# Kernel tuning notes

Measured on AMD Instinct MI355X. Metric: run time of the kernel, lower is better.

## Reference

```python
import jax, jax.numpy as jnp
import numpy as np

N_HEADS = 16
HEAD_SIZE = 64
N_EMB = 1024
BLOCK = 2048
B, T = 2, 2048

def setup_inputs() -> dict:
    key = jax.random.key(0)
    ks = jax.random.split(key, 6)
    s = 0.02
    x = jax.random.normal(ks[0], (B, T, N_EMB), dtype=jnp.float32)
    # per-head projection weights, stacked: [H, C, hs] (no bias, per module)
    Wq = jax.random.normal(ks[1], (N_HEADS, N_EMB, HEAD_SIZE), dtype=jnp.float32) * s
    Wk = jax.random.normal(ks[2], (N_HEADS, N_EMB, HEAD_SIZE), dtype=jnp.float32) * s
    Wv = jax.random.normal(ks[3], (N_HEADS, N_EMB, HEAD_SIZE), dtype=jnp.float32) * s
    # output projection: Linear(n_heads*head_size -> n_embedding), with bias
    Wo = jax.random.normal(ks[4], (N_HEADS * HEAD_SIZE, N_EMB), dtype=jnp.float32) * s
    bo = jax.random.normal(ks[5], (N_EMB,), dtype=jnp.float32) * s
    return {"x": x, "Wq": Wq, "Wk": Wk, "Wv": Wv, "Wo": Wo, "bo": bo}

def reference(x, Wq, Wk, Wv, Wo, bo):
    # x: [B,T,C]; projections per head -> [B,H,T,hs]
    q = jnp.einsum('btc,hcd->bhtd', x, Wq)
    k = jnp.einsum('btc,hcd->bhtd', x, Wk)
    v = jnp.einsum('btc,hcd->bhtd', x, Wv)
    scale = 1.0 / jnp.sqrt(jnp.asarray(HEAD_SIZE, dtype=x.dtype))
    scores = jnp.einsum('bhtd,bhsd->bhts', q, k) * scale  # [B,H,T,T]
    Tq = x.shape[1]
    causal = jnp.tril(jnp.ones((Tq, Tq), dtype=bool))
    scores = jnp.where(causal, scores, jnp.asarray(-jnp.inf, dtype=scores.dtype))
    attn = jax.nn.softmax(scores, axis=-1)  # dropout in eval mode (identity)
    out = jnp.einsum('bhts,bhsd->bhtd', attn, v)  # [B,H,T,hs]
    # concat heads along last dim (matches torch.cat order over head list)
    out = out.transpose(0, 2, 1, 3).reshape(x.shape[0], Tq, N_HEADS * HEAD_SIZE)
    return out @ Wo + bo
```

## Files before the change

kernel.cpp:

```cpp
#include <hip/hip_runtime.h>


typedef short v8s __attribute__((ext_vector_type(8)));
typedef float v4f __attribute__((ext_vector_type(4)));

#define DEVI __device__ __forceinline__

#define B_SZ 2
#define T_SEQ 2048
#define NH 16
#define HS 64
#define CEMB 1024
#define MROWS (B_SZ * T_SEQ)
#define KSZ 1024
#define SCALE_Q 0.18033688011112042f

DEVI unsigned short f2bf(float f) {
  union { float f; unsigned u; } c; c.f = f;
  unsigned u = c.u;
  unsigned r = (u + 0x7FFFu + ((u >> 16) & 1u)) >> 16;
  return (unsigned short)r;
}

DEVI float exp2_fast(float x) {
  float r;
  asm("v_exp_f32 %0, %1" : "=v"(r) : "v"(x));
  return r;
}

DEVI unsigned cvt_pk_bf16(float lo, float hi) {
  unsigned r;
  asm("v_cvt_pk_bf16_f32 %0, %1, %2" : "=v"(r) : "v"(lo), "v"(hi));
  return r;
}

DEVI void gload_lds16(const void* g, void* l) {
  __builtin_amdgcn_global_load_lds(
      (const __attribute__((address_space(1))) void*)g,
      (__attribute__((address_space(3))) void*)l, 16, 0, 0);
}

DEVI int xcd_swz(int bid, int nwg) {
  int q = nwg >> 3;
  return (bid & 7) * q + (bid >> 3);
}

__global__ __launch_bounds__(256, 4) void prep_kernel(
    const float* __restrict__ x, const float* __restrict__ Wq,
    const float* __restrict__ Wk, const float* __restrict__ Wv,
    const float* __restrict__ Wo, unsigned short* __restrict__ xb,
    unsigned short* __restrict__ Wt, unsigned short* __restrict__ Wot) {
  int bid = blockIdx.x;
  if (bid < 2048) {
    int i = bid * 2048 + threadIdx.x * 8;
    float4 a = *(const float4*)(x + i);
    float4 b = *(const float4*)(x + i + 4);
    ushort4 o0, o1;
    o0.x = f2bf(a.x); o0.y = f2bf(a.y); o0.z = f2bf(a.z); o0.w = f2bf(a.w);
    o1.x = f2bf(b.x); o1.y = f2bf(b.y); o1.z = f2bf(b.z); o1.w = f2bf(b.w);
    *(ushort4*)(xb + i) = o0;
    *(ushort4*)(xb + i + 4) = o1;
    return;
  }
  __shared__ float tile[32][33];
  const float* in; unsigned short* out;
  int C, bx, by;
  if (bid < 5120) {
    int b2 = bid - 2048;
    int widx = b2 >> 10, rem = b2 & 1023;
    in = (widx == 0 ? Wq : (widx == 1 ? Wk : Wv));
    int z = rem >> 6;
    bx = rem & 1; by = (rem >> 1) & 31;
    C = 64;
    in += (size_t)z * 1024 * 64;
    out = Wt + ((size_t)widx << 20) + (size_t)z * 1024 * 64;
  } else {
    int rem = bid - 5120;
    C = 1024;
    bx = rem & 31; by = rem >> 5;
    in = Wo; out = Wot;
  }
  int c0 = bx * 32, r0 = by * 32;
  int tx = threadIdx.x & 31, ty = threadIdx.x >> 5;
#pragma unroll
  for (int j = 0; j < 4; ++j)
    tile[ty + j * 8][tx] = in[(size_t)(r0 + ty + j * 8) * C + c0 + tx];
  __syncthreads();
#pragma unroll
  for (int j = 0; j < 4; ++j)
    out[(size_t)(c0 + ty + j * 8) * 1024 + r0 + tx] = f2bf(tile[tx][ty + j * 8]);
}

template <int MODE>
__global__ __launch_bounds__(256, 3) void gemm_bt(
    const unsigned short* __restrict__ A, const unsigned short* __restrict__ Bt,
    void* __restrict__ Cout, const float* __restrict__ bias, int nbx) {
  __shared__ __align__(16) unsigned short As[3][128 * 32];
  __shared__ __align__(16) unsigned short Bs[3][128 * 32];

  const int tid = threadIdx.x;
  const int lane = tid & 63, w = tid >> 6;
  const int wm = w >> 1, wn = w & 1;
  const int lr = lane & 15, lg = lane >> 4;

  const int wg = xcd_swz(blockIdx.x, gridDim.x);
  const int mb = (wg / nbx) * 128, nb = (wg % nbx) * 128;

  v4f acc[4][4];
  v4f zero = {0.f, 0.f, 0.f, 0.f};
#pragma unroll
  for (int i = 0; i < 4; ++i)
#pragma unroll
    for (int j = 0; j < 4; ++j) acc[i][j] = zero;

  const int srow = lane >> 2;
  const int sgcol = ((lane & 3) ^ (srow & 3)) * 8;
  const unsigned short* gA = A + (size_t)(mb + w * 32 + srow) * KSZ + sgcol;
  const unsigned short* gB = Bt + (size_t)(nb + w * 32 + srow) * KSZ + sgcol;
  unsigned short* lA = &As[0][0] + w * 1024;
  unsigned short* lB = &Bs[0][0] + w * 1024;

#define STAGE_G(buf, kb)                                        \
  do {                                                          \
    gload_lds16(gA + (kb), lA + (buf) * 4096);                  \
    gload_lds16(gA + (kb) + 16 * KSZ, lA + (buf) * 4096 + 512); \
    gload_lds16(gB + (kb), lB + (buf) * 4096);                  \
    gload_lds16(gB + (kb) + 16 * KSZ, lB + (buf) * 4096 + 512); \
  } while (0)

  STAGE_G(0, 0);
  STAGE_G(1, 32);
  STAGE_G(2, 64);

  const int NT = KSZ / 32;
  for (int t = 0; t < NT; ++t) {
    asm volatile("s_waitcnt vmcnt(8)" ::: "memory");
    __builtin_amdgcn_s_barrier();

    const int buf = t % 3;
    v8s af[4], bfr[4];
#pragma unroll
    for (int i = 0; i < 4; ++i) {
      int ra = wm * 64 + i * 16 + lr, rb = wn * 64 + i * 16 + lr;
      af[i]  = *(const v8s*)&As[buf][ra * 32 + ((lg ^ (lr & 3)) << 3)];
      bfr[i] = *(const v8s*)&Bs[buf][rb * 32 + ((lg ^ (lr & 3)) << 3)];
    }
#pragma unroll
    for (int i = 0; i < 4; ++i)
#pragma unroll
      for (int j = 0; j < 4; ++j)
        acc[i][j] = __builtin_amdgcn_mfma_f32_16x16x32_bf16(af[i], bfr[j], acc[i][j], 0, 0, 0);

    asm volatile("s_waitcnt lgkmcnt(0)" ::: "memory");
    __builtin_amdgcn_s_barrier();
    if (t + 3 < NT) STAGE_G(buf, (t + 3) * 32);
  }
#undef STAGE_G

#pragma unroll
  for (int i = 0; i < 4; ++i) {
    int mrow0 = mb + wm * 64 + i * 16 + lg * 4;
#pragma unroll
    for (int j = 0; j < 4; ++j) {
      int ncol = nb + wn * 64 + j * 16 + lr;
      if (MODE == 0) {
        int p = ncol >> 10, rem = ncol & 1023, h = rem >> 6, d = rem & 63;
        float sc = (p == 0) ? SCALE_Q : 1.0f;
        unsigned short* out = (unsigned short*)Cout;
#pragma unroll
        for (int r = 0; r < 4; ++r) {
          int mrow = mrow0 + r;
          int b = mrow >> 11, t = mrow & 2047;
          size_t off;
          if (p < 2)
            off = ((size_t)((p * B_SZ + b) * NH + h) * T_SEQ + t) * HS + d;
          else
            off = (size_t)(2 * B_SZ * NH) * T_SEQ * HS +
                  ((size_t)(b * NH + h) * HS + d) * T_SEQ + t;
          out[off] = f2bf(acc[i][j][r] * sc);
        }
      } else {
        float* out = (float*)Cout;
        float bv = bias[ncol];
#pragma unroll
        for (int r = 0; r < 4; ++r)
          out[(size_t)(mrow0 + r) * CEMB + ncol] = acc[i][j][r] + bv;
      }
    }
  }
}

__global__ __launch_bounds__(512, 4) void attn_kernel(
    const unsigned short* __restrict__ Qg, const unsigned short* __restrict__ Kg,
    const unsigned short* __restrict__ Vtg, unsigned short* __restrict__ Yg) {
  __shared__ __align__(16) unsigned char lds[32 * 1024];
  unsigned char* KsB = lds;
  unsigned char* VtB = lds + 16384;

  const int tid = threadIdx.x;
  const int lane = tid & 63, w = tid >> 6;
  const int lr = lane & 15, lg = lane >> 4;
  const int qc = 15 - (blockIdx.x >> 5);
  const int bh = blockIdx.x & 31;

  const unsigned short* Qbase = Qg + (size_t)bh * T_SEQ * HS;
  const unsigned short* Kbase = Kg + (size_t)bh * T_SEQ * HS;
  const unsigned short* Vtbase = Vtg + (size_t)bh * T_SEQ * HS;

  const int ks_row = tid >> 3, ks_cb = tid & 7;
  const int kLds0 = ks_row * 128 + ((ks_cb ^ (ks_row & 7)) << 4);
  const unsigned short* Kg0 = Kbase + ks_row * HS + ks_cb * 8;
  const int vs_d = tid >> 4, vs_m = tid & 15;
  const int vLds0 = vs_d * 256 + ((vs_m ^ (vs_d & 15)) << 4);
  const int vbt = ((vs_m >> 2) << 4) + ((vs_m & 3) << 2);
  const unsigned short* Vg0 = Vtbase + (size_t)vs_d * T_SEQ + vbt;

  v8s qA[2];
  {
    const unsigned short* qrow = Qbase + (size_t)(qc * 128 + w * 16 + lr) * HS;
    qA[0] = *(const v8s*)(qrow + lg * 8);
    qA[1] = *(const v8s*)(qrow + 32 + lg * 8);
  }

  v4f O[4];
  v4f zero = {0.f, 0.f, 0.f, 0.f};
#pragma unroll
  for (int d = 0; d < 4; ++d) O[d] = zero;
  float mrun = -1e30f, lrun = 0.f;

  int4 gK0 = *(const int4*)(Kg0);
  int4 gK1 = *(const int4*)(Kg0 + 4096);
  int2 vlo0 = *(const int2*)(Vg0);
  int2 vhi0 = *(const int2*)(Vg0 + 64);
  int2 vlo1 = *(const int2*)(Vg0 + 32 * T_SEQ);
  int2 vhi1 = *(const int2*)(Vg0 + 32 * T_SEQ + 64);

  for (int t = 0; t <= qc; ++t) {
    __syncthreads();
    *(int4*)(KsB + kLds0) = gK0;
    *(int4*)(KsB + kLds0 + 8192) = gK1;
    {
      int4 v0; v0.x = vlo0.x; v0.y = vlo0.y; v0.z = vhi0.x; v0.w = vhi0.y;
      int4 v1; v1.x = vlo1.x; v1.y = vlo1.y; v1.z = vhi1.x; v1.w = vhi1.y;
      *(int4*)(VtB + vLds0) = v0;
      *(int4*)(VtB + vLds0 + 8192) = v1;
    }
    __syncthreads();
    if (t < qc) {
      const unsigned short* kp = Kg0 + (t + 1) * (128 * HS);
      gK0 = *(const int4*)kp;
      gK1 = *(const int4*)(kp + 4096);
      const unsigned short* vp = Vg0 + (t + 1) * 128;
      vlo0 = *(const int2*)(vp);
      vhi0 = *(const int2*)(vp + 64);
      vlo1 = *(const int2*)(vp + 32 * T_SEQ);
      vhi1 = *(const int2*)(vp + 32 * T_SEQ + 64);
    }

    const int cflim = (t == qc) ? w : 7;

    v4f S[8];
    __builtin_amdgcn_s_setprio(1);
#pragma unroll
    for (int cf = 0; cf < 8; ++cf) {
      if (cf <= cflim) {
        S[cf] = zero;
#pragma unroll
        for (int ks = 0; ks < 2; ++ks) {
          int srow = cf * 16 + lr;
          v8s kb = *(const v8s*)(KsB + srow * 128 +
                                 ((((ks << 2) + lg) ^ (lr & 7)) << 4));
          S[cf] = __builtin_amdgcn_mfma_f32_16x16x32_bf16(kb, qA[ks], S[cf], 0, 0, 0);
        }
      } else {
        S[cf] = (v4f){-1e30f, -1e30f, -1e30f, -1e30f};
      }
    }
    __builtin_amdgcn_s_setprio(0);

    if (t == qc) {
#pragma unroll
      for (int cf = 0; cf < 8; ++cf)
        if (cf == w) {
#pragma unroll
          for (int r = 0; r < 4; ++r)
            if (lg * 4 + r > lr) S[cf][r] = -1e30f;
        }
    }

    float mx = -1e30f;
#pragma unroll
    for (int cf = 0; cf < 8; ++cf)
#pragma unroll
      for (int r = 0; r < 4; ++r) mx = fmaxf(mx, S[cf][r]);
    mx = fmaxf(mx, __shfl_xor(mx, 16));
    mx = fmaxf(mx, __shfl_xor(mx, 32));

    if (!__all(mx - mrun <= 8.0f)) {
      float mn = fmaxf(mrun, mx);
      float alpha = exp2_fast(mrun - mn);
      mrun = mn;
      lrun *= alpha;
#pragma unroll
      for (int df = 0; df < 4; ++df)
#pragma unroll
        for (int r = 0; r < 4; ++r) O[df][r] *= alpha;
    }

    float sum = 0.f;
#pragma unroll
    for (int cf = 0; cf < 8; ++cf)
#pragma unroll
      for (int r = 0; r < 4; ++r) {
        float p = exp2_fast(S[cf][r] - mrun);
        S[cf][r] = p;
        sum += p;
      }
    sum += __shfl_xor(sum, 16);
    sum += __shfl_xor(sum, 32);
    lrun += sum;

    unsigned pk0[8], pk1[8];
#pragma unroll
    for (int cf = 0; cf < 8; ++cf) {
      pk0[cf] = cvt_pk_bf16(S[cf][0], S[cf][1]);
      pk1[cf] = cvt_pk_bf16(S[cf][2], S[cf][3]);
    }

    __builtin_amdgcn_s_setprio(1);
#pragma unroll
    for (int c = 0; c < 4; ++c) {
      if (t != qc || c <= w) {
        union { unsigned u[4]; v8s s; } pu;
        pu.u[0] = pk0[c]; pu.u[1] = pk1[c];
        pu.u[2] = pk0[c + 4]; pu.u[3] = pk1[c + 4];
        v8s pa = pu.s;
#pragma unroll
        for (int df = 0; df < 4; ++df) {
          int d = df * 16 + lr;
          v8s va = *(const v8s*)(VtB + d * 256 +
                                 ((((c << 2) + lg) ^ lr) << 4));
          O[df] = __builtin_amdgcn_mfma_f32_16x16x32_bf16(va, pa, O[df], 0, 0, 0);
        }
      }
    }
    __builtin_amdgcn_s_setprio(0);
  }

  float invl = 1.0f / lrun;
  int tq = qc * 128 + w * 16 + lr;
  int b = bh >> 4, h = bh & 15;
  size_t ybase = ((size_t)b * T_SEQ + tq) * (NH * HS) + h * 64;
#pragma unroll
  for (int df = 0; df < 4; ++df) {
    ushort4 o4;
    o4.x = f2bf(O[df][0] * invl);
    o4.y = f2bf(O[df][1] * invl);
    o4.z = f2bf(O[df][2] * invl);
    o4.w = f2bf(O[df][3] * invl);
    *(ushort4*)(Yg + ybase + df * 16 + lg * 4) = o4;
  }
}

extern "C" void kernel_launch(void* const* d_in, const int* in_sizes, int n_in,
                              void* d_out, int out_size, void* d_ws, size_t ws_size,
                              hipStream_t stream) {
  (void)in_sizes; (void)n_in; (void)out_size; (void)ws_size;
  const float* x  = (const float*)d_in[0];
  const float* Wq = (const float*)d_in[1];
  const float* Wk = (const float*)d_in[2];
  const float* Wv = (const float*)d_in[3];
  const float* Wo = (const float*)d_in[4];
  const float* bo = (const float*)d_in[5];

  unsigned char* ws = (unsigned char*)d_ws;
  unsigned short* xb  = (unsigned short*)(ws);
  unsigned short* Wt  = (unsigned short*)(ws + (8u << 20));
  unsigned short* Wot = (unsigned short*)(ws + (14u << 20));
  unsigned short* qkv = (unsigned short*)(ws + (16u << 20));
  unsigned short* Y   = (unsigned short*)(ws + (40u << 20));

  prep_kernel<<<dim3(6144), 256, 0, stream>>>(x, Wq, Wk, Wv, Wo, xb, Wt, Wot);

  gemm_bt<0><<<dim3(768), 256, 0, stream>>>(xb, Wt, qkv, nullptr, 24);

  const unsigned short* Qp = qkv;
  const unsigned short* Kp = qkv + (size_t)B_SZ * NH * T_SEQ * HS;
  const unsigned short* Vtp = qkv + (size_t)2 * B_SZ * NH * T_SEQ * HS;
  attn_kernel<<<dim3(512), 512, 0, stream>>>(Qp, Kp, Vtp, Y);

  gemm_bt<1><<<dim3(256), 256, 0, stream>>>(Y, Wot, d_out, bo, 8);
}
```

Before: 110.8 us.

## Replace QKV projection GEMM with 256x256-tile, 8-wave ping-pong pipelined kernel

Result: slower. 123.5 us (+11.5%).

```diff
diff --git a/kernel.cpp b/kernel.cpp
--- a/kernel.cpp
+++ b/kernel.cpp
@@ -91,10 +91,182 @@
     out[(size_t)(c0 + ty + j * 8) * 1024 + r0 + tx] = f2bf(tile[tx][ty + j * 8]);
 }
 
-template <int MODE>
-__global__ __launch_bounds__(256, 3) void gemm_bt(
+DEVI void stage_half(const unsigned short* gbase, unsigned char* lbase,
+                     int kt, int slot, int h) {
+  const unsigned short* g = gbase + (size_t)h * (128 * KSZ) + kt * 64;
+  unsigned char* l = lbase + slot * 32768 + h * 16384;
+  gload_lds16(g, l);
+  gload_lds16(g + 64 * KSZ, l + 8192);
+}
+
+template <int MQ>
+DEVI void read_aq(const unsigned char* rA, int lg, int lr, v8s (&a)[4][2]) {
+  const unsigned char* p = rA + MQ * 8192 + lr * 128;
+#pragma unroll
+  for (int m = 0; m < 4; ++m)
+#pragma unroll
+    for (int ks = 0; ks < 2; ++ks)
+      a[m][ks] = *(const v8s*)(p + m * 2048 +
+                               ((((ks << 2) + lg) ^ (lr & 7)) << 4));
+}
+
+template <int NQ>
+DEVI void read_bq(const unsigned char* rB, int lg, int lr, v8s (&b)[4][2]) {
+  const unsigned char* p = rB + NQ * 4096 + lr * 128;
+#pragma unroll
+  for (int j = 0; j < 2; ++j)
+#pragma unroll
+    for (int ks = 0; ks < 2; ++ks)
+      b[NQ * 2 + j][ks] = *(const v8s*)(p + j * 2048 +
+                                        ((((ks << 2) + lg) ^ (lr & 7)) << 4));
+}
+
+template <int MQ, int NQ>
+DEVI void mfma_quad(const v8s (&a)[4][2], const v8s (&b)[4][2],
+                    v4f (&acc)[8][4]) {
+  __builtin_amdgcn_s_setprio(1);
+#pragma unroll
+  for (int m = 0; m < 4; ++m)
+#pragma unroll
+    for (int j = 0; j < 2; ++j)
+#pragma unroll
+      for (int ks = 0; ks < 2; ++ks)
+        acc[MQ * 4 + m][NQ * 2 + j] = __builtin_amdgcn_mfma_f32_16x16x32_bf16(
+            a[m][ks], b[NQ * 2 + j][ks], acc[MQ * 4 + m][NQ * 2 + j], 0, 0, 0);
+  __builtin_amdgcn_s_setprio(0);
+}
+
+__global__ __launch_bounds__(512, 2) void gemm256(
     const unsigned short* __restrict__ A, const unsigned short* __restrict__ Bt,
-    void* __restrict__ Cout, const float* __restrict__ bias, int nbx) {
+    unsigned short* __restrict__ Cout, int nbx) {
+  __shared__ __align__(16) unsigned char lds[131072];
+
+  const int tid = threadIdx.x;
+  const int lane = tid & 63, w = tid >> 6;
+  const int wm = w >> 2, wn = w & 3;
+  const int lr = lane & 15, lg = lane >> 4;
+  const int wg = xcd_swz(blockIdx.x, gridDim.x);
+  const int mb = (wg / nbx) * 256, nb = (wg % nbx) * 256;
+
+  v4f acc[8][4];
+  v4f zero = {0.f, 0.f, 0.f, 0.f};
+#pragma unroll
+  for (int i = 0; i < 8; ++i)
+#pragma unroll
+    for (int j = 0; j < 4; ++j) acc[i][j] = zero;
+
+  const int ts_row = tid >> 3;
+  const int gch = (tid & 7) ^ (ts_row & 7);
+  const unsigned short* gA = A + (size_t)(mb + ts_row) * KSZ + gch * 8;
+  const unsigned short* gB = Bt + (size_t)(nb + ts_row) * KSZ + gch * 8;
+  unsigned char* lA = lds + w * 1024;
+  unsigned char* lB = lds + 65536 + w * 1024;
+
+  const unsigned char* rA = lds + wm * 16384;
+  const unsigned char* rB = lds + 65536 + (wn >> 1) * 16384 + (wn & 1) * 8192;
+
+  v8s aq[4][2], bq[4][2];
+
+  stage_half(gA, lA, 0, 0, 0);
+  stage_half(gA, lA, 0, 0, 1);
+  stage_half(gB, lB, 0, 0, 0);
+  stage_half(gB, lB, 0, 0, 1);
+  stage_half(gA, lA, 1, 1, 0);
+
+  for (int it = 0; it < 8; ++it) {
+    const int c = 2 * it;
+    asm volatile("s_waitcnt vmcnt(2)" ::: "memory");
+    __builtin_amdgcn_s_barrier();
+
+    read_aq<0>(rA, lg, lr, aq);
+    read_bq<0>(rB, lg, lr, bq);
+    stage_half(gA, lA, c + 1, 1, 1);
+    __builtin_amdgcn_s_barrier();
+    asm volatile("s_waitcnt lgkmcnt(0)" ::: "memory");
+    mfma_quad<0, 0>(aq, bq, acc);
+    __builtin_amdgcn_s_barrier();
+
+    read_bq<1>(rB, lg, lr, bq);
+    stage_half(gB, lB, c + 1, 1, 0);
+    __builtin_amdgcn_s_barrier();
+    asm volatile("s_waitcnt lgkmcnt(0)" ::: "memory");
+    mfma_quad<0, 1>(aq, bq, acc);
+    __builtin_amdgcn_s_barrier();
+
+    read_aq<1>(rA, lg, lr, aq);
+    stage_half(gB, lB, c + 1, 1, 1);
+    __builtin_amdgcn_s_barrier();
+    asm volatile("s_waitcnt lgkmcnt(0)" ::: "memory");
+    mfma_quad<1, 0>(aq, bq, acc);
+    __builtin_amdgcn_s_barrier();
+
+    if (it < 7) stage_half(gA, lA, c + 2, 0, 0);
+    __builtin_amdgcn_s_barrier();
+    mfma_quad<1, 1>(aq, bq, acc);
+    __builtin_amdgcn_s_barrier();
+
+    if (it == 7) {
+      asm volatile("s_waitcnt vmcnt(0)" ::: "memory");
+    } else {
+      asm volatile("s_waitcnt vmcnt(2)" ::: "memory");
+    }
+    __builtin_amdgcn_s_barrier();
+
+    read_aq<0>(rA + 32768, lg, lr, aq);
+    read_bq<0>(rB + 32768, lg, lr, bq);
+    if (it < 7) stage_half(gA, lA, c + 2, 0, 1);
+    __builtin_amdgcn_s_barrier();
+    asm volatile("s_waitcnt lgkmcnt(0)" ::: "memory");
+    mfma_quad<0, 0>(aq, bq, acc);
+    __builtin_amdgcn_s_barrier();
+
+    read_bq<1>(rB + 32768, lg, lr, bq);
+    if (it < 7) stage_half(gB, lB, c + 2, 0, 0);
+    __builtin_amdgcn_s_barrier();
+    asm volatile("s_waitcnt lgkmcnt(0)" ::: "memory");
+    mfma_quad<0, 1>(aq, bq, acc);
+    __builtin_amdgcn_s_barrier();
+
+    read_aq<1>(rA + 32768, lg, lr, aq);
+    if (it < 7) stage_half(gB, lB, c + 2, 0, 1);
+    __builtin_amdgcn_s_barrier();
+    asm volatile("s_waitcnt lgkmcnt(0)" ::: "memory");
+    mfma_quad<1, 0>(aq, bq, acc);
+    __builtin_amdgcn_s_barrier();
+
+    if (it < 7) stage_half(gA, lA, c + 3, 1, 0);
+    __builtin_amdgcn_s_barrier();
+    mfma_quad<1, 1>(aq, bq, acc);
+    __builtin_amdgcn_s_barrier();
+  }
+
+#pragma unroll
+  for (int i = 0; i < 8; ++i) {
+    int mrow0 = mb + wm * 128 + i * 16 + lg * 4;
+#pragma unroll
+    for (int j = 0; j < 4; ++j) {
+      int ncol = nb + wn * 64 + j * 16 + lr;
+      int p = ncol >> 10, rem = ncol & 1023, h = rem >> 6, d = rem & 63;
+      float sc = (p == 0) ? SCALE_Q : 1.0f;
+#pragma unroll
+      for (int r = 0; r < 4; ++r) {
+        int mrow = mrow0 + r;
+        int b = mrow >> 11, t = mrow & 2047;
+        size_t off;
+        if (p < 2)
+          off = ((size_t)((p * B_SZ + b) * NH + h) * T_SEQ + t) * HS + d;
+        else
+          off = (size_t)(2 * B_SZ * NH) * T_SEQ * HS +
+                ((size_t)(b * NH + h) * HS + d) * T_SEQ + t;
+        Cout[off] = f2bf(acc[i][j][r] * sc);
+      }
+    }
+  }
+}
+
+__global__ __launch_bounds__(256, 3) void gemm_proj(
+    const unsigned short* __restrict__ A, const unsigned short* __restrict__ Bt,
+    float* __restrict__ Cout, const float* __restrict__ bias, int nbx) {
   __shared__ __align__(16) unsigned short As[3][128 * 32];
   __shared__ __align__(16) unsigned short Bs[3][128 * 32];
 
@@ -163,29 +335,10 @@
 #pragma unroll
     for (int j = 0; j < 4; ++j) {
       int ncol = nb + wn * 64 + j * 16 + lr;
-      if (MODE == 0) {
-        int p = ncol >> 10, rem = ncol & 1023, h = rem >> 6, d = rem & 63;
-        float sc = (p == 0) ? SCALE_Q : 1.0f;
-        unsigned short* out = (unsigned short*)Cout;
-#pragma unroll
-        for (int r = 0; r < 4; ++r) {
-          int mrow = mrow0 + r;
-          int b = mrow >> 11, t = mrow & 2047;
-          size_t off;
-          if (p < 2)
-            off = ((size_t)((p * B_SZ + b) * NH + h) * T_SEQ + t) * HS + d;
-          else
-            off = (size_t)(2 * B_SZ * NH) * T_SEQ * HS +
-                  ((size_t)(b * NH + h) * HS + d) * T_SEQ + t;
-          out[off] = f2bf(acc[i][j][r] * sc);
-        }
-      } else {
-        float* out = (float*)Cout;
-        float bv = bias[ncol];
-#pragma unroll
-        for (int r = 0; r < 4; ++r)
-          out[(size_t)(mrow0 + r) * CEMB + ncol] = acc[i][j][r] + bv;
-      }
+      float bv = bias[ncol];
+#pragma unroll
+      for (int r = 0; r < 4; ++r)
+        Cout[(size_t)(mrow0 + r) * CEMB + ncol] = acc[i][j][r] + bv;
     }
   }
 }
@@ -382,12 +535,12 @@
 
   prep_kernel<<<dim3(6144), 256, 0, stream>>>(x, Wq, Wk, Wv, Wo, xb, Wt, Wot);
 
-  gemm_bt<0><<<dim3(768), 256, 0, stream>>>(xb, Wt, qkv, nullptr, 24);
+  gemm256<<<dim3(192), 512, 0, stream>>>(xb, Wt, qkv, 12);
 
   const unsigned short* Qp = qkv;
   const unsigned short* Kp = qkv + (size_t)B_SZ * NH * T_SEQ * HS;
   const unsigned short* Vtp = qkv + (size_t)2 * B_SZ * NH * T_SEQ * HS;
   attn_kernel<<<dim3(512), 512, 0, stream>>>(Qp, Kp, Vtp, Y);
 
-  gemm_bt<1><<<dim3(256), 256, 0, stream>>>(Y, Wot, d_out, bo, 8);
-}
+  gemm_proj<<<dim3(256), 256, 0, stream>>>(Y, Wot, (float*)d_out, bo, 8);
+}
```
